# Performance work log

Hardware: AMD Instinct MI355X
Metric: run time of the kernel (lower is better)

The kernel has to match this reference:

```python
import jax, jax.numpy as jnp
import numpy as np

B, IN_SHAPE, EXP_SHAPE, HID, NB_CLASSES = 64, 10000, 53, 1500, 2048


def setup_inputs() -> dict:
    key = jax.random.key(0)
    ks = jax.random.split(key, 8)
    gos = jax.random.uniform(ks[0], (B, IN_SHAPE), dtype=jnp.float32)
    exp_x = jax.random.uniform(ks[1], (B, EXP_SHAPE), dtype=jnp.float32)
    # FlatModel params (torch Linear: y = x @ W.T + b; store pre-transposed)
    W1 = jax.random.normal(ks[2], (IN_SHAPE, HID), dtype=jnp.float32) * (1.0 / np.sqrt(IN_SHAPE))
    b1 = jnp.zeros((HID,), dtype=jnp.float32)
    W2 = jax.random.normal(ks[3], (HID + EXP_SHAPE, NB_CLASSES), dtype=jnp.float32) * (1.0 / np.sqrt(HID + EXP_SHAPE))
    b2 = jnp.zeros((NB_CLASSES,), dtype=jnp.float32)
    # HPO adjacency (non-trainable buffer in the original; values in [0,1))
    hpo_matrix = jax.random.uniform(ks[4], (NB_CLASSES, NB_CLASSES), dtype=jnp.float32)
    return {"gos": gos, "exp_x": exp_x, "W1": W1, "b1": b1, "W2": W2, "b2": b2, "hpo_matrix": hpo_matrix}


def reference(gos, exp_x, W1, b1, W2, b2, hpo_matrix):
    # FlatModel (eval mode: dropout is identity). torch F.gelu default = exact erf gelu.
    h = jax.nn.gelu(gos @ W1 + b1, approximate=False)          # (B, HID)
    x = jnp.concatenate([h, exp_x], axis=1)                     # (B, HID+EXP)
    flat = jax.nn.sigmoid(x @ W2 + b2)                          # (B, C)
    # HPOLayer + permute + MaxPool1d(C): out[b,j] = max_i flat[b,j] * M[i,j]
    out = jnp.max(flat[:, None, :] * hpo_matrix[None, :, :], axis=1)  # (B, C)
    return out
```

## Files before the change

### kernel.cpp

```cpp
#include <hip/hip_runtime.h>
#include <math.h>

#define B64 64
#define IN_SH 10000
#define EXP_SH 53
#define HID 1500
#define NPAD1 1536
#define NBC 2048
#define K2 1553
#define KS1 40
#define KST1 8
#define KS2 13
#define KST2 4
#define CMCH 32
#define WLDS 640

using short8  = __attribute__((ext_vector_type(8))) short;
using floatx4 = __attribute__((ext_vector_type(4))) float;
using uintx4  = __attribute__((ext_vector_type(4))) unsigned int;

__device__ __forceinline__ unsigned short f2bf(float f) {
    unsigned u = __float_as_uint(f);
    u += 0x7fffu + ((u >> 16) & 1u);
    return (unsigned short)(u >> 16);
}


__global__ __launch_bounds__(256) void prep_k(const float* __restrict__ g,
                                              unsigned short* __restrict__ gosBf,
                                              const float* __restrict__ M,
                                              float* __restrict__ cm,
                                              float* __restrict__ accz) {
    int bi = blockIdx.x;
    if (bi < 320) {
        int t    = bi * 256 + threadIdx.x;
        int lane = t & 63;
        int sgrp = (t >> 6) & 3;
        int step = t >> 8;
        int q    = lane >> 4;
        int l15  = lane & 15;
        int b    = sgrp * 16 + l15;
        int k0   = step * 32 + q * 8;
        const float* p = g + (size_t)b * IN_SH + k0;
        unsigned int o[4];
        #pragma unroll
        for (int i = 0; i < 4; i++) {
            float lo = (k0 + 2 * i     < IN_SH) ? p[2 * i]     : 0.f;
            float hi = (k0 + 2 * i + 1 < IN_SH) ? p[2 * i + 1] : 0.f;
            o[i] = (unsigned)f2bf(lo) | ((unsigned)f2bf(hi) << 16);
        }
        uintx4 v; v.x = o[0]; v.y = o[1]; v.z = o[2]; v.w = o[3];
        *(uintx4*)(gosBf + (size_t)t * 8) = v;
    } else if (bi < 576) {
        int ci = bi - 320;
        int j  = (ci & 7) * 256 + threadIdx.x;
        int i0 = (ci >> 3) * 64;
        float m = 0.0f;
        #pragma unroll 16
        for (int i = i0; i < i0 + 64; i++)
            m = fmaxf(m, M[(size_t)i * NBC + j]);
        cm[(ci >> 3) * NBC + j] = m;
    } else {
        int t = (bi - 576) * 256 + threadIdx.x;
        floatx4 z = (floatx4){0.f, 0.f, 0.f, 0.f};
        #pragma unroll
        for (int i = 0; i < 28; i++)
            *(floatx4*)(accz + (size_t)(i * 2048 + t) * 4) = z;
    }
}

__device__ __forceinline__ void load_b4(const unsigned short* __restrict__ bf,
                                        int stg, uintx4 bv[4]) {
    #pragma unroll
    for (int s = 0; s < 4; s++)
        bv[s] = *(const uintx4*)(bf + (size_t)(stg * 4 + s) * 512);
}

template<int KSTEPS>
__device__ __forceinline__ void gemm_core(
    const float* __restrict__ W, const unsigned short* __restrict__ Bf,
    float* __restrict__ accbuf, int N, int K, int ldw, int bx, int by, int tid,
    float* __restrict__ ldsw)
{
    int lane = tid & 63;
    int q    = lane >> 4;
    int l15  = lane & 15;
    int n0   = bx * 64 + 16 * (tid >> 6);
    int k0   = by * (KSTEPS * 32);
    bool fast = (n0 + 16 <= N) && (k0 + KSTEPS * 32 <= K);
    int kl  = lane >> 2;
    int c4  = (lane & 3) * 4;

    const unsigned short* bf = Bf + (size_t)(by * KSTEPS * 4) * 512 + (size_t)lane * 8;

    floatx4 acc[4];
    #pragma unroll
    for (int s = 0; s < 4; s++) acc[s] = (floatx4){0.f, 0.f, 0.f, 0.f};

    floatx4 g[2][2];

    #define GLB(st, slot)                                                        \
        {                                                                        \
            int kb_ = k0 + (st) * 32;                                            \
            _Pragma("unroll")                                                    \
            for (int i_ = 0; i_ < 2; i_++) {                                     \
                int kg_ = kb_ + kl + 16 * i_;                                    \
                if (fast) {                                                      \
                    g[slot][i_] = *(const floatx4*)(W + (size_t)kg_ * ldw + n0 + c4); \
                } else {                                                         \
                    _Pragma("unroll")                                            \
                    for (int j_ = 0; j_ < 4; j_++)                               \
                        g[slot][i_][j_] = (kg_ < K && n0 + c4 + j_ < N)          \
                            ? W[(size_t)kg_ * ldw + n0 + c4 + j_] : 0.f;         \
                }                                                                \
            }                                                                    \
        }
    #define LWR(buf, slot)                                                       \
        {                                                                        \
            _Pragma("unroll")                                                    \
            for (int i_ = 0; i_ < 2; i_++)                                       \
                *(floatx4*)(ldsw + (buf) * WLDS + (kl + 16 * i_) * 20 + c4) = g[slot][i_]; \
        }

    GLB(0, 0);
    if (KSTEPS > 1) GLB(1, 1);
    LWR(0, 0);

    uintx4 bv[2][4];
    load_b4(bf, 0, bv[0]);
    if (KSTEPS > 1) load_b4(bf, 1, bv[1]);

    #pragma unroll
    for (int st = 0; st < KSTEPS; st++) {
        const int s = st & 1;
        const float* lb = ldsw + s * WLDS;

        short8 af;
        #pragma unroll
        for (int j = 0; j < 8; j++)
            af[j] = (short)f2bf(lb[(q * 8 + j) * 20 + l15]);

        uintx4 bt[4];
        if (st + 2 < KSTEPS) {
            GLB(st + 2, s);
            load_b4(bf, st + 2, bt);
        }

        #pragma unroll
        for (int m = 0; m < 4; m++) {
            short8 bf8 = __builtin_bit_cast(short8, bv[s][m]);
            acc[m] = __builtin_amdgcn_mfma_f32_16x16x32_bf16(af, bf8, acc[m], 0, 0, 0);
        }

        if (st + 1 < KSTEPS) LWR(1 - s, 1 - s);
        if (st + 2 < KSTEPS) {
            #pragma unroll
            for (int m = 0; m < 4; m++) bv[s][m] = bt[m];
        }
    }
    #undef GLB
    #undef LWR

    int nrow = n0 + q * 4;
    #pragma unroll
    for (int s = 0; s < 4; s++) {
        #pragma unroll
        for (int rr = 0; rr < 4; rr++)
            atomicAdd(&accbuf[(size_t)(nrow + rr) * 64 + s * 16 + l15], acc[s][rr]);
    }
}

__global__ __launch_bounds__(256) void gemm1_k(
    const float* __restrict__ W1, const unsigned short* __restrict__ gosBf,
    float* __restrict__ hpre)
{
    __shared__ float lds[4 * 2 * WLDS];
    gemm_core<KST1>(W1, gosBf, hpre, HID, IN_SH, HID, blockIdx.x, blockIdx.y,
                    threadIdx.x, lds + (threadIdx.x >> 6) * (2 * WLDS));
}

__global__ __launch_bounds__(256) void gemm2_k(
    const float* __restrict__ W2, const unsigned short* __restrict__ Xf,
    float* __restrict__ logits)
{
    __shared__ float lds[4 * 2 * WLDS];
    gemm_core<KST2>(W2, Xf, logits, NBC, K2, NBC, blockIdx.x, blockIdx.y,
                    threadIdx.x, lds + (threadIdx.x >> 6) * (2 * WLDS));
}

__global__ __launch_bounds__(256) void combine1(
    const float* __restrict__ hpre, const float* __restrict__ b1,
    const float* __restrict__ expx, unsigned short* __restrict__ Xf)
{
    int t    = blockIdx.x * 256 + threadIdx.x;
    int lane = t & 63;
    int sgrp = (t >> 6) & 3;
    int step = t >> 8;
    int q    = lane >> 4;
    int l15  = lane & 15;
    int b    = sgrp * 16 + l15;
    int kb   = step * 32 + q * 8;
    unsigned int o[4];
    #pragma unroll
    for (int i = 0; i < 4; i++) {
        unsigned int lohi[2];
        #pragma unroll
        for (int h = 0; h < 2; h++) {
            int n = kb + 2 * i + h;
            float v = 0.f;
            if (n < HID) {
                float s = hpre[(size_t)n * 64 + b] + b1[n];
                v = 0.5f * s * (1.0f + erff(s * 0.70710678118654752f));
            } else if (n < HID + EXP_SH) {
                v = expx[b * EXP_SH + (n - HID)];
            }
            lohi[h] = f2bf(v);
        }
        o[i] = lohi[0] | (lohi[1] << 16);
    }
    uintx4 v; v.x = o[0]; v.y = o[1]; v.z = o[2]; v.w = o[3];
    *(uintx4*)(Xf + (size_t)t * 8) = v;
}

__global__ __launch_bounds__(256) void final_k(
    const float* __restrict__ logits, const float* __restrict__ b2,
    const float* __restrict__ cm, float* __restrict__ out)
{
    int idx = blockIdx.x * 256 + threadIdx.x;
    int b = idx & 63;
    int j = idx >> 6;
    float s = logits[(size_t)j * 64 + b] + b2[j];
    float sig = 1.0f / (1.0f + expf(-s));
    float m = 0.f;
    #pragma unroll
    for (int c = 0; c < CMCH; c++) m = fmaxf(m, cm[c * NBC + j]);
    out[(size_t)b * NBC + j] = sig * m;
}

extern "C" void kernel_launch(void* const* d_in, const int* in_sizes, int n_in,
                              void* d_out, int out_size, void* d_ws, size_t ws_size,
                              hipStream_t stream) {
    const float* gos  = (const float*)d_in[0];
    const float* expx = (const float*)d_in[1];
    const float* W1   = (const float*)d_in[2];
    const float* b1   = (const float*)d_in[3];
    const float* W2   = (const float*)d_in[4];
    const float* b2   = (const float*)d_in[5];
    const float* hpo  = (const float*)d_in[6];
    float* out = (float*)d_out;

    char* ws = (char*)d_ws;
    unsigned short* gosBf = (unsigned short*)ws;
    float* hpre   = (float*)(ws + 1310720);
    float* logits = (float*)(ws + 1310720 + 393216);
    unsigned short* Xf = (unsigned short*)(ws + 1310720 + 393216 + 524288);
    float* cm = (float*)(ws + 1310720 + 393216 + 524288 + 212992);

    prep_k<<<584, 256, 0, stream>>>(gos, gosBf, hpo, cm, hpre);

    gemm1_k<<<dim3(NPAD1 / 64, KS1), 256, 0, stream>>>(W1, gosBf, hpre);

    combine1<<<52, 256, 0, stream>>>(hpre, b1, expx, Xf);

    gemm2_k<<<dim3(NBC / 64, KS2), 256, 0, stream>>>(W2, Xf, logits);

    final_k<<<(B64 * NBC) / 256, 256, 0, stream>>>(logits, b2, cm, out);
}
```

Measured before the change: 162.3 us.

## Fuse GELU/concat/bf16 packing into gemm2 prologue via shared-memory fragments

```diff
diff --git a/kernel.cpp b/kernel.cpp
--- a/kernel.cpp
+++ b/kernel.cpp
@@ -78,7 +78,7 @@
 
 template<int KSTEPS>
 __device__ __forceinline__ void gemm_core(
-    const float* __restrict__ W, const unsigned short* __restrict__ Bf,
+    const float* __restrict__ W, const unsigned short* __restrict__ Bfc,
     float* __restrict__ accbuf, int N, int K, int ldw, int bx, int by, int tid,
     float* __restrict__ ldsw)
 {
@@ -91,7 +91,7 @@
     int kl  = lane >> 2;
     int c4  = (lane & 3) * 4;
 
-    const unsigned short* bf = Bf + (size_t)(by * KSTEPS * 4) * 512 + (size_t)lane * 8;
+    const unsigned short* bf = Bfc + (size_t)lane * 8;
 
     floatx4 acc[4];
     #pragma unroll
@@ -175,51 +175,54 @@
     float* __restrict__ hpre)
 {
     __shared__ float lds[4 * 2 * WLDS];
-    gemm_core<KST1>(W1, gosBf, hpre, HID, IN_SH, HID, blockIdx.x, blockIdx.y,
+    gemm_core<KST1>(W1, gosBf + (size_t)blockIdx.y * (KST1 * 4) * 512,
+                    hpre, HID, IN_SH, HID, blockIdx.x, blockIdx.y,
                     threadIdx.x, lds + (threadIdx.x >> 6) * (2 * WLDS));
 }
 
 __global__ __launch_bounds__(256) void gemm2_k(
-    const float* __restrict__ W2, const unsigned short* __restrict__ Xf,
+    const float* __restrict__ W2, const float* __restrict__ hpre,
+    const float* __restrict__ b1, const float* __restrict__ expx,
     float* __restrict__ logits)
 {
     __shared__ float lds[4 * 2 * WLDS];
-    gemm_core<KST2>(W2, Xf, logits, NBC, K2, NBC, blockIdx.x, blockIdx.y,
-                    threadIdx.x, lds + (threadIdx.x >> 6) * (2 * WLDS));
-}
-
-__global__ __launch_bounds__(256) void combine1(
-    const float* __restrict__ hpre, const float* __restrict__ b1,
-    const float* __restrict__ expx, unsigned short* __restrict__ Xf)
-{
-    int t    = blockIdx.x * 256 + threadIdx.x;
-    int lane = t & 63;
-    int sgrp = (t >> 6) & 3;
-    int step = t >> 8;
-    int q    = lane >> 4;
-    int l15  = lane & 15;
-    int b    = sgrp * 16 + l15;
-    int kb   = step * 32 + q * 8;
-    unsigned int o[4];
-    #pragma unroll
-    for (int i = 0; i < 4; i++) {
-        unsigned int lohi[2];
-        #pragma unroll
-        for (int h = 0; h < 2; h++) {
-            int n = kb + 2 * i + h;
-            float v = 0.f;
-            if (n < HID) {
-                float s = hpre[(size_t)n * 64 + b] + b1[n];
-                v = 0.5f * s * (1.0f + erff(s * 0.70710678118654752f));
-            } else if (n < HID + EXP_SH) {
-                v = expx[b * EXP_SH + (n - HID)];
+    __shared__ unsigned short bfrag[KST2 * 4 * 64 * 8];
+    int tid = threadIdx.x;
+    int by  = blockIdx.y;
+
+    #pragma unroll
+    for (int it = 0; it < 4; it++) {
+        int tl   = it * 256 + tid;
+        int stg  = tl >> 8;
+        int sgrp = (tl >> 6) & 3;
+        int lane = tl & 63;
+        int b    = sgrp * 16 + (lane & 15);
+        int nb   = (by * 4 + stg) * 32 + (lane >> 4) * 8;
+        unsigned int o[4];
+        #pragma unroll
+        for (int i = 0; i < 4; i++) {
+            unsigned int lohi[2];
+            #pragma unroll
+            for (int h = 0; h < 2; h++) {
+                int n = nb + 2 * i + h;
+                float v = 0.f;
+                if (n < HID) {
+                    float s = hpre[(size_t)n * 64 + b] + b1[n];
+                    v = 0.5f * s * (1.0f + erff(s * 0.70710678118654752f));
+                } else if (n < HID + EXP_SH) {
+                    v = expx[b * EXP_SH + (n - HID)];
+                }
+                lohi[h] = f2bf(v);
             }
-            lohi[h] = f2bf(v);
-        }
-        o[i] = lohi[0] | (lohi[1] << 16);
-    }
-    uintx4 v; v.x = o[0]; v.y = o[1]; v.z = o[2]; v.w = o[3];
-    *(uintx4*)(Xf + (size_t)t * 8) = v;
+            o[i] = lohi[0] | (lohi[1] << 16);
+        }
+        uintx4 v; v.x = o[0]; v.y = o[1]; v.z = o[2]; v.w = o[3];
+        *(uintx4*)(bfrag + (size_t)tl * 8) = v;
+    }
+    __syncthreads();
+
+    gemm_core<KST2>(W2, bfrag, logits, NBC, K2, NBC, blockIdx.x, by,
+                    tid, lds + (tid >> 6) * (2 * WLDS));
 }
 
 __global__ __launch_bounds__(256) void final_k(
@@ -253,16 +256,13 @@
     unsigned short* gosBf = (unsigned short*)ws;
     float* hpre   = (float*)(ws + 1310720);
     float* logits = (float*)(ws + 1310720 + 393216);
-    unsigned short* Xf = (unsigned short*)(ws + 1310720 + 393216 + 524288);
-    float* cm = (float*)(ws + 1310720 + 393216 + 524288 + 212992);
+    float* cm     = (float*)(ws + 1310720 + 393216 + 524288);
 
     prep_k<<<584, 256, 0, stream>>>(gos, gosBf, hpo, cm, hpre);
 
     gemm1_k<<<dim3(NPAD1 / 64, KS1), 256, 0, stream>>>(W1, gosBf, hpre);
 
-    combine1<<<52, 256, 0, stream>>>(hpre, b1, expx, Xf);
-
-    gemm2_k<<<dim3(NBC / 64, KS2), 256, 0, stream>>>(W2, Xf, logits);
+    gemm2_k<<<dim3(NBC / 64, KS2), 256, 0, stream>>>(W2, hpre, b1, expx, logits);
 
     final_k<<<(B64 * NBC) / 256, 256, 0, stream>>>(logits, b2, cm, out);
 }
```

After: 167.8 us. +3.4%, slower.
